# Optimization experiments

Hardware: AMD Instinct MI355X
Metric: run time of the kernel (lower is better)

The kernel has to match this reference:

```python
import jax, jax.numpy as jnp
import numpy as np


def _window(Hs, Ws):
    # Gaussian blending window, sigma = min(Hs, Ws)/4 (matches generate_window)
    y = jnp.linspace(-Hs / 2.0, Hs / 2.0, Hs)
    x = jnp.linspace(-Ws / 2.0, Ws / 2.0, Ws)
    Y, X = jnp.meshgrid(y, x, indexing='ij')
    sigma = min(Hs, Ws) / 4.0
    return jnp.exp(-0.5 * ((X / sigma) ** 2 + (Y / sigma) ** 2)).astype(jnp.float32)


def _conv_tile(seg, psf_l):
    # seg: [B, H, W] tile; psf_l: [L, Hp, Wp] -> [B, L, H, W]
    # Faithful to simulate_image; the fftshift/ifftshift pair in the frequency
    # domain cancels in the product, so it is omitted (identical math).
    B, H, W = seg.shape
    L, Hp, Wp = psf_l.shape
    tph, tpw = Hp, Wp          # target padding (padded size = H+Hp, W+Wp)
    pph, ppw = H, W            # psf padding
    seg_p = jnp.pad(seg, ((0, 0), (tph // 2, tph - tph // 2), (tpw // 2, tpw - tpw // 2)))
    psf_p = jnp.pad(psf_l, ((0, 0), (pph // 2, pph - pph // 2), (ppw // 2, ppw - ppw // 2)))
    F_seg = jnp.fft.fft2(jnp.fft.ifftshift(seg_p, axes=(-2, -1)))
    F_psf = jnp.fft.fft2(jnp.fft.ifftshift(psf_p, axes=(-2, -1)))
    conv = jnp.fft.fftshift(jnp.fft.ifft2(F_seg[:, None] * F_psf[None]), axes=(-2, -1)).real
    return conv[:, :, tph // 2: tph // 2 + H, tpw // 2: tpw // 2 + W]


def _sv_forward(target_images, psfs, overlap):
    # render_sensor_ideal_sv (pixel_map = identity) -> rot90
    im = jnp.rot90(target_images, k=1, axes=(-2, -1))
    # prep_psfs: [L,P,Hp,Wp] -> [L,n,n,Hp,Wp], transpose grid, rot90 each PSF
    L, P, Hp, Wp = psfs.shape
    n = int(round(P ** 0.5))
    ps = psfs.reshape(L, n, n, Hp, Wp).transpose(0, 2, 1, 3, 4)
    ps = jnp.rot90(ps, k=1, axes=(-2, -1))
    B, _, H, W = im.shape
    Hs, Ws = H // n, W // n
    out = jnp.zeros((B, L, H, W), jnp.float32)
    norm = jnp.zeros((H, W), jnp.float32)
    for i in range(n):            # small fixed grid (n*n = 16 tiles)
        for j in range(n):
            h0 = max(0, i * Hs - overlap // 2)
            h1 = min(H, (i + 1) * Hs + overlap // 2)
            w0 = max(0, j * Ws - overlap // 2)
            w1 = min(W, (j + 1) * Ws + overlap // 2)
            seg = im[:, 0, h0:h1, w0:w1]
            win = _window(h1 - h0, w1 - w0)
            cap = _conv_tile(seg, ps[:, i, j]) * win      # all L layers batched
            out = out.at[:, :, h0:h1, w0:w1].add(cap)
            norm = norm.at[h0:h1, w0:w1].add(win)
    out = out / jnp.maximum(norm, 1e-12)[None, None]
    out = jnp.nan_to_num(out, nan=0.0)
    return jnp.rot90(out, k=-1, axes=(-2, -1))  # rotate_back


def setup_inputs() -> dict:
    key = jax.random.key(0)
    k1, k2 = jax.random.split(key)
    target_images = jax.random.uniform(k1, (2, 1, 2048, 2048), dtype=jnp.float32)
    psfs = jax.random.uniform(k2, (3, 16, 128, 128), dtype=jnp.float32)
    return {"target_images": target_images, "psfs": psfs, "overlap": 64}


def reference(target_images, psfs, overlap):
    return _sv_forward(target_images, psfs, int(overlap))
```

## Files before the change

### kernel.cpp

```cpp
#include <hip/hip_runtime.h>

typedef __attribute__((ext_vector_type(8))) short short8;
typedef __attribute__((ext_vector_type(4))) float f32x4;

#define IMH 2048
#define IMW 2048
#define NB 2
#define NL 3
#define NT 4
#define HS 512
#define OV2 32
#define PH 128

#define PSTRIDE 272
#define PATCH_ROWS 96
#define NDI 10

__device__ __forceinline__ ushort f2bf(float f) {
  unsigned u = __float_as_uint(f);
  return (ushort)((u + 0x7FFFu + ((u >> 16) & 1u)) >> 16);
}

__global__ void build_J16(const float* __restrict__ tgt, ushort* __restrict__ J16) {
  int idx = blockIdx.x * 256 + threadIdx.x;
  if (idx >= NB * IMH * IMW) return;
  int c = idx & (IMW - 1);
  int r = (idx >> 11) & (IMH - 1);
  int b = idx >> 22;
  J16[idx] = f2bf(tgt[((size_t)(b * IMH) + r) * IMW + (IMW - 1 - c)]);
}

__global__ void build_Bfrag(const float* __restrict__ psfs, uint4* __restrict__ Bf) {
  int idx = blockIdx.x * 256 + threadIdx.x;
  if (idx >= 48 * 128 * NDI * 64) return;
  int ln = idx & 63;
  int di = (idx >> 6) % NDI;
  int q  = (idx / (64 * NDI)) & 127;
  int pf = idx / (64 * NDI * 128);
  int tj = pf & 3, ti = (pf >> 2) & 3, l = pf >> 4;
  const float* col = psfs + ((size_t)((l * 16 + tj * 4 + ti) * PH + q)) * PH;
  int n = ln & 15, h = ln >> 4;
  int p0 = 16 * di + n - 8 * h;
  ushort v[8];
  #pragma unroll
  for (int i = 0; i < 8; ++i) {
    int p = p0 - i;
    v[i] = (p >= 0 && p < PH) ? f2bf(col[PH - 1 - p]) : (ushort)0;
  }
  uint4 o;
  o.x = (unsigned)v[0] | ((unsigned)v[1] << 16);
  o.y = (unsigned)v[2] | ((unsigned)v[3] << 16);
  o.z = (unsigned)v[4] | ((unsigned)v[5] << 16);
  o.w = (unsigned)v[6] | ((unsigned)v[7] << 16);
  Bf[idx] = o;
}

#define MFMA16(a, bfr, c) __builtin_amdgcn_mfma_f32_16x16x32_bf16((a), (bfr), (c), 0, 0, 0)
#define SBAR() __builtin_amdgcn_sched_barrier(0)

__global__ __launch_bounds__(256, 3)
void conv_mfma(const ushort* __restrict__ J16, const short8* __restrict__ Bfrag,
               float* __restrict__ out) {
  __shared__ __align__(16) ushort patch[PATCH_ROWS * PSTRIDE];

  const int tid  = threadIdx.x;
  const int lane = tid & 63;
  const int xs   = tid >> 6;
  const int n    = lane & 15;
  const int hq   = lane >> 4;

  const int f = blockIdx.x + (blockIdx.y << 5);
  const int g = f >> 5, wi = f & 31;
  const int x0 = ((((g & 3) << 3) + (wi & 7)) << 6);
  const int y0 = ((((g >> 2) << 2) + (wi >> 3)) << 7);
  const int bl = blockIdx.z;
  const int b = bl / NL, l = bl - NL * b;

  const int tylo = (y0 > OV2 ? (y0 - OV2) : 0) / HS;
  const int tyhi = min(NT - 1, (y0 + 127 + OV2) / HS);
  const int txlo = (x0 > OV2 ? (x0 - OV2) : 0) / HS;
  const int txhi = min(NT - 1, (x0 + 63 + OV2) / HS);

  f32x4 facc[8] = {};

  for (int ti = tylo; ti <= tyhi; ++ti) {
    const int h0 = max(0, ti * HS - OV2);
    const int h1 = min(IMH, (ti + 1) * HS + OV2);
    for (int tj = txlo; tj <= txhi; ++tj) {
      const int w0 = max(0, tj * HS - OV2);
      const int w1 = min(IMW, (tj + 1) * HS + OV2);

      const short8* __restrict__ Bt =
          Bfrag + (size_t)((l * 4 + ti) * 4 + tj) * (128 * NDI * 64) + lane;

      const int xw = x0 + (xs << 4);
      const int qminw = xw + 65 - w1;
      const int qmaxw = xw + 79 - w0;

      f32x4 acc[8] = {};

      #pragma unroll 1
      for (int qlo = 0; qlo < 128; qlo += 32) {
        const int rrlo = 97 - qlo;
        __syncthreads();
        const int rbase = x0 - 64 + rrlo;
        const int cbase = y0 - 64;
        #pragma unroll 4
        for (int item = tid; item < 95 * 32; item += 256) {
          const int slot = item >> 5;
          const int c    = item & 31;
          const int rg   = rbase + slot;
          const int cg   = cbase + (c << 3);
          uint4 v = {0u, 0u, 0u, 0u};
          if (rg >= w0 && rg < w1 && cg >= h0 && (cg + 8) <= h1)
            v = *(const uint4*)(J16 + ((size_t)b << 22) + ((size_t)rg << 11) + cg);
          *(uint4*)&patch[slot * PSTRIDE + (((c ^ (slot & 3))) << 3)] = v;
        }
        __syncthreads();

        int s2 = qminw - qlo; if (s2 < 0) s2 = 0;
        int e2 = qmaxw - qlo + 1; if (e2 > 32) e2 = 32;
        if (s2 >= e2) continue;

        const int sbase = (xs << 4) + n + 128 - rrlo;

        short8 B[NDI], AP[4];

        const int q0 = qlo + s2;
        {
          const short8* __restrict__ Bp0 = Bt + (size_t)q0 * (NDI * 64);
          #pragma unroll
          for (int d = 0; d < NDI; ++d) B[d] = Bp0[d << 6];
          const int row0 = sbase - q0;
          const ushort* __restrict__ ar0 =
              patch + row0 * PSTRIDE + ((hq ^ (row0 & 3)) << 3);
          AP[0] = *(const short8*)(ar0);
          AP[1] = *(const short8*)(ar0 + 32);
          AP[2] = *(const short8*)(ar0 + 64);
          AP[3] = *(const short8*)(ar0 + 96);
        }

        auto qstep = [&](int q, int qn) {
          const int row = sbase - q;
          const ushort* __restrict__ ar =
              patch + row * PSTRIDE + ((hq ^ (row & 3)) << 3);
          short8 AH[4];
          AH[0] = *(const short8*)(ar + 128);
          AH[1] = *(const short8*)(ar + 160);
          AH[2] = *(const short8*)(ar + 192);
          AH[3] = *(const short8*)(ar + 224);
          const short8* __restrict__ Bp = Bt + (size_t)qn * (NDI * 64);
          int rowp = sbase - qn; if (rowp < 0) rowp = 0;
          const ushort* __restrict__ arp =
              patch + rowp * PSTRIDE + ((hq ^ (rowp & 3)) << 3);
          SBAR();
          acc[0] = MFMA16(AP[0], B[8], acc[0]);
          acc[1] = MFMA16(AP[0], B[9], acc[1]);
          acc[2] = MFMA16(AP[1], B[8], acc[2]);
          acc[3] = MFMA16(AP[1], B[9], acc[3]);
          acc[4] = MFMA16(AP[2], B[8], acc[4]);
          acc[5] = MFMA16(AP[2], B[9], acc[5]);
          acc[6] = MFMA16(AP[3], B[8], acc[6]);
          acc[7] = MFMA16(AP[3], B[9], acc[7]);
          SBAR();
          B[8] = Bp[8 << 6]; B[9] = Bp[9 << 6];
          SBAR();
          acc[0] = MFMA16(AP[1], B[6], acc[0]);
          acc[1] = MFMA16(AP[1], B[7], acc[1]);
          acc[2] = MFMA16(AP[2], B[6], acc[2]);
          acc[3] = MFMA16(AP[2], B[7], acc[3]);
          acc[4] = MFMA16(AP[3], B[6], acc[4]);
          acc[5] = MFMA16(AP[3], B[7], acc[5]);
          acc[6] = MFMA16(AH[0], B[6], acc[6]);
          acc[7] = MFMA16(AH[0], B[7], acc[7]);
          SBAR();
          B[6] = Bp[6 << 6]; B[7] = Bp[7 << 6];
          SBAR();
          acc[0] = MFMA16(AP[2], B[4], acc[0]);
          acc[1] = MFMA16(AP[2], B[5], acc[1]);
          acc[2] = MFMA16(AP[3], B[4], acc[2]);
          acc[3] = MFMA16(AP[3], B[5], acc[3]);
          acc[4] = MFMA16(AH[0], B[4], acc[4]);
          acc[5] = MFMA16(AH[0], B[5], acc[5]);
          acc[6] = MFMA16(AH[1], B[4], acc[6]);
          acc[7] = MFMA16(AH[1], B[5], acc[7]);
          SBAR();
          B[4] = Bp[4 << 6]; B[5] = Bp[5 << 6];
          SBAR();
          acc[0] = MFMA16(AP[3], B[2], acc[0]);
          acc[1] = MFMA16(AP[3], B[3], acc[1]);
          acc[2] = MFMA16(AH[0], B[2], acc[2]);
          acc[3] = MFMA16(AH[0], B[3], acc[3]);
          acc[4] = MFMA16(AH[1], B[2], acc[4]);
          acc[5] = MFMA16(AH[1], B[3], acc[5]);
          acc[6] = MFMA16(AH[2], B[2], acc[6]);
          acc[7] = MFMA16(AH[2], B[3], acc[7]);
          SBAR();
          B[2] = Bp[2 << 6]; B[3] = Bp[3 << 6];
          AP[0] = *(const short8*)(arp);
          AP[1] = *(const short8*)(arp + 32);
          AP[2] = *(const short8*)(arp + 64);
          AP[3] = *(const short8*)(arp + 96);
          SBAR();
          acc[0] = MFMA16(AH[0], B[0], acc[0]);
          acc[1] = MFMA16(AH[0], B[1], acc[1]);
          acc[2] = MFMA16(AH[1], B[0], acc[2]);
          acc[3] = MFMA16(AH[1], B[1], acc[3]);
          acc[4] = MFMA16(AH[2], B[0], acc[4]);
          acc[5] = MFMA16(AH[2], B[1], acc[5]);
          acc[6] = MFMA16(AH[3], B[0], acc[6]);
          acc[7] = MFMA16(AH[3], B[1], acc[7]);
          SBAR();
          B[0] = Bp[0 << 6]; B[1] = Bp[1 << 6];
          SBAR();
        };

        #pragma unroll 1
        for (int q2 = s2; q2 < e2; ++q2) {
          const int q = qlo + q2;
          qstep(q, min(q + 1, 127));
        }
      }

      const int Sh = h1 - h0, Sw = w1 - w0;
      const float sig = 0.25f * (float)min(Sh, Sw);
      const float c2 = 0.5f / (sig * sig);
      const float stepy = (float)Sh / (float)(Sh - 1);
      const float stepx = (float)Sw / (float)(Sw - 1);
      float wx[4];
      #pragma unroll
      for (int r = 0; r < 4; ++r) {
        const int x = x0 + (xs << 4) + (hq << 2) + r;
        const float xv = -0.5f * (float)Sw + (float)(x - w0) * stepx;
        wx[r] = (x >= w0 && x < w1) ? __expf(-xv * xv * c2) : 0.0f;
      }
      #pragma unroll
      for (int s = 0; s < 8; ++s) {
        const int y = y0 + (s << 4) + n;
        const float yv = -0.5f * (float)Sh + (float)(y - h0) * stepy;
        const float wy = (y >= h0 && y < h1) ? __expf(-yv * yv * c2) : 0.0f;
        #pragma unroll
        for (int r = 0; r < 4; ++r) facc[s][r] += wy * wx[r] * acc[s][r];
      }
    }
  }

  f32x4 nacc[8] = {};
  for (int ti = tylo; ti <= tyhi; ++ti) {
    const int h0 = max(0, ti * HS - OV2);
    const int h1 = min(IMH, (ti + 1) * HS + OV2);
    for (int tj = txlo; tj <= txhi; ++tj) {
      const int w0 = max(0, tj * HS - OV2);
      const int w1 = min(IMW, (tj + 1) * HS + OV2);
      const int Sh = h1 - h0, Sw = w1 - w0;
      const float sig = 0.25f * (float)min(Sh, Sw);
      const float c2 = 0.5f / (sig * sig);
      const float stepy = (float)Sh / (float)(Sh - 1);
      const float stepx = (float)Sw / (float)(Sw - 1);
      float wx[4];
      #pragma unroll
      for (int r = 0; r < 4; ++r) {
        const int x = x0 + (xs << 4) + (hq << 2) + r;
        const float xv = -0.5f * (float)Sw + (float)(x - w0) * stepx;
        wx[r] = (x >= w0 && x < w1) ? __expf(-xv * xv * c2) : 0.0f;
      }
      #pragma unroll
      for (int s = 0; s < 8; ++s) {
        const int y = y0 + (s << 4) + n;
        const float yv = -0.5f * (float)Sh + (float)(y - h0) * stepy;
        const float wy = (y >= h0 && y < h1) ? __expf(-yv * yv * c2) : 0.0f;
        #pragma unroll
        for (int r = 0; r < 4; ++r) nacc[s][r] += wy * wx[r];
      }
    }
  }
  #pragma unroll
  for (int s = 0; s < 8; ++s) {
    const int y = y0 + (s << 4) + n;
    #pragma unroll
    for (int r = 0; r < 4; ++r) {
      const int x = x0 + (xs << 4) + (hq << 2) + r;
      out[(((size_t)(b * NL + l) << 11) + x) * IMW + (IMW - 1 - y)] =
          facc[s][r] / fmaxf(nacc[s][r], 1e-12f);
    }
  }
}

extern "C" void kernel_launch(void* const* d_in, const int* in_sizes, int n_in,
                              void* d_out, int out_size, void* d_ws, size_t ws_size,
                              hipStream_t stream) {
  const float* tgt  = (const float*)d_in[0];
  const float* psfs = (const float*)d_in[1];
  ushort* J16 = (ushort*)d_ws;
  short8* Bf  = (short8*)((char*)d_ws + (size_t)NB * IMH * IMW * 2);
  float* o = (float*)d_out;

  build_J16<<<dim3((NB * IMH * IMW + 255) / 256), 256, 0, stream>>>(tgt, J16);
  build_Bfrag<<<dim3((48 * 128 * NDI * 64 + 255) / 256), 256, 0, stream>>>(
      psfs, (uint4*)Bf);
  conv_mfma<<<dim3(32, 16, NB * NL), 256, 0, stream>>>(J16, Bf, o);
}
```

Baseline: 1.651 ms.

## Skip MFMAs for row strips outside tile and remap block-to-tile order

Adds a partial-tile path that works out which 32-row strips of the 128-row output block fall inside the current overlap tile and issues MFMAs only for those strips. Fully covered blocks keep the original unrolled step. It also remaps blockIdx to output coordinates so neighbouring blocks in launch order share different tile regions, which may change cache locality. The partial path uses runtime-predicated MFMA groups, which could hurt scheduling. Only border blocks benefit.

```diff
diff --git a/kernel.cpp b/kernel.cpp
--- a/kernel.cpp
+++ b/kernel.cpp
@@ -69,8 +69,9 @@
   const int n    = lane & 15;
   const int hq   = lane >> 4;
 
-  const int f = blockIdx.x + (blockIdx.y << 5);
-  const int g = f >> 5, wi = f & 31;
+  const int c  = blockIdx.x & 7;
+  const int g  = (c << 1) | (blockIdx.y >> 3);
+  const int wi = (blockIdx.x >> 3) | ((blockIdx.y & 7) << 2);
   const int x0 = ((((g & 3) << 3) + (wi & 7)) << 6);
   const int y0 = ((((g >> 2) << 2) + (wi >> 3)) << 7);
   const int bl = blockIdx.z;
@@ -86,6 +87,9 @@
   for (int ti = tylo; ti <= tyhi; ++ti) {
     const int h0 = max(0, ti * HS - OV2);
     const int h1 = min(IMH, (ti + 1) * HS + OV2);
+    const int splo = max(0, (h0 - y0) / 32);
+    const int sphi = min(3, (h1 - 1 - y0) / 32);
+    const bool fullS = (splo == 0) & (sphi == 3);
     for (int tj = txlo; tj <= txhi; ++tj) {
       const int w0 = max(0, tj * HS - OV2);
       const int w1 = min(IMW, (tj + 1) * HS + OV2);
@@ -108,13 +112,13 @@
         #pragma unroll 4
         for (int item = tid; item < 95 * 32; item += 256) {
           const int slot = item >> 5;
-          const int c    = item & 31;
+          const int cc   = item & 31;
           const int rg   = rbase + slot;
-          const int cg   = cbase + (c << 3);
+          const int cg   = cbase + (cc << 3);
           uint4 v = {0u, 0u, 0u, 0u};
           if (rg >= w0 && rg < w1 && cg >= h0 && (cg + 8) <= h1)
             v = *(const uint4*)(J16 + ((size_t)b << 22) + ((size_t)rg << 11) + cg);
-          *(uint4*)&patch[slot * PSTRIDE + (((c ^ (slot & 3))) << 3)] = v;
+          *(uint4*)&patch[slot * PSTRIDE + (((cc ^ (slot & 3))) << 3)] = v;
         }
         __syncthreads();
 
@@ -140,7 +144,7 @@
           AP[3] = *(const short8*)(ar0 + 96);
         }
 
-        auto qstep = [&](int q, int qn) {
+        auto qstepF = [&](int q, int qn) {
           const int row = sbase - q;
           const ushort* __restrict__ ar =
               patch + row * PSTRIDE + ((hq ^ (row & 3)) << 3);
@@ -215,10 +219,66 @@
           SBAR();
         };
 
-        #pragma unroll 1
-        for (int q2 = s2; q2 < e2; ++q2) {
-          const int q = qlo + q2;
-          qstep(q, min(q + 1, 127));
+        auto qstepP = [&](int q, int qn) {
+          const int row = sbase - q;
+          const ushort* __restrict__ ar =
+              patch + row * PSTRIDE + ((hq ^ (row & 3)) << 3);
+          short8 AH[4];
+          AH[0] = *(const short8*)(ar + 128);
+          AH[1] = *(const short8*)(ar + 160);
+          AH[2] = *(const short8*)(ar + 192);
+          AH[3] = *(const short8*)(ar + 224);
+          const short8* __restrict__ Bp = Bt + (size_t)qn * (NDI * 64);
+          int rowp = sbase - qn; if (rowp < 0) rowp = 0;
+          const ushort* __restrict__ arp =
+              patch + rowp * PSTRIDE + ((hq ^ (rowp & 3)) << 3);
+          SBAR();
+          #pragma unroll
+          for (int k = 0; k < 5; ++k) {
+            if (splo <= 0 && 0 <= sphi) {
+              const short8 Aj = (k < 4) ? AP[k] : AH[k - 4];
+              acc[0] = MFMA16(Aj, B[8 - (k << 1)], acc[0]);
+              acc[1] = MFMA16(Aj, B[9 - (k << 1)], acc[1]);
+            }
+            if (splo <= 1 && 1 <= sphi) {
+              const short8 Aj = (1 + k < 4) ? AP[1 + k] : AH[k - 3];
+              acc[2] = MFMA16(Aj, B[8 - (k << 1)], acc[2]);
+              acc[3] = MFMA16(Aj, B[9 - (k << 1)], acc[3]);
+            }
+            if (splo <= 2 && 2 <= sphi) {
+              const short8 Aj = (2 + k < 4) ? AP[2 + k] : AH[k - 2];
+              acc[4] = MFMA16(Aj, B[8 - (k << 1)], acc[4]);
+              acc[5] = MFMA16(Aj, B[9 - (k << 1)], acc[5]);
+            }
+            if (splo <= 3 && 3 <= sphi) {
+              const short8 Aj = (3 + k < 4) ? AP[3 + k] : AH[k - 1];
+              acc[6] = MFMA16(Aj, B[8 - (k << 1)], acc[6]);
+              acc[7] = MFMA16(Aj, B[9 - (k << 1)], acc[7]);
+            }
+            B[8 - (k << 1)] = Bp[(8 - (k << 1)) << 6];
+            B[9 - (k << 1)] = Bp[(9 - (k << 1)) << 6];
+            if (k == 3) {
+              AP[0] = *(const short8*)(arp);
+              AP[1] = *(const short8*)(arp + 32);
+              AP[2] = *(const short8*)(arp + 64);
+              AP[3] = *(const short8*)(arp + 96);
+            }
+            SBAR();
+          }
+        };
+
+        if (fullS) {
+          #pragma unroll 1
+          for (int q2 = s2; q2 < e2; ++q2) {
+            const int q = qlo + q2;
+            qstepF(q, min(q + 1, 127));
+          }
+        } else {
+          #pragma unroll 1
+          for (int q2 = s2; q2 < e2; ++q2) {
+            const int q = qlo + q2;
+            qstepP(q, min(q + 1, 127));
+          }
         }
       }
 
```

New measurement: 2.260 ms. 36.9% more time.
